# Performance work log

Measured on AMD Instinct MI355X. Metric: run time of the kernel, lower is better.

## Reference

```python
import jax, jax.numpy as jnp
import numpy as np

H, DH, D, S, B = 8, 64, 512, 512, 2
EPS = 1e-5

def _trop_linear(x, W):
    # y[..., o] = max_i (x[..., i] + W[o, i])
    return jnp.max(x[..., None, :] + W, axis=-1)

def _layer_norm(x, gamma, beta):
    mu = jnp.mean(x, axis=-1, keepdims=True)
    var = jnp.mean((x - mu) ** 2, axis=-1, keepdims=True)
    return (x - mu) * jax.lax.rsqrt(var + EPS) * gamma + beta

def setup_inputs() -> dict:
    key = jax.random.key(0)
    ks = jax.random.split(key, 8)
    sc = lambda fan_in: 1.0 / np.sqrt(fan_in)
    return {
        "h":   jax.random.normal(ks[0], (S, B, D), jnp.float32),
        "Wq":  jax.random.normal(ks[1], (H * DH, D), jnp.float32) * sc(D),
        "Wkv": jax.random.normal(ks[2], (2 * H * DH, D), jnp.float32) * sc(D),
        "Wqt": jax.random.normal(ks[3], (DH, DH), jnp.float32),
        "Wkt": jax.random.normal(ks[4], (DH, DH), jnp.float32),
        "Wvt": jax.random.normal(ks[5], (DH, DH), jnp.float32),
        "lam": jnp.ones((1, 1, D), jnp.float32),
        "Wo":  jax.random.normal(ks[6], (D, H * DH), jnp.float32) * sc(H * DH),
        "gamma": jnp.ones((D,), jnp.float32),
        "beta":  jnp.zeros((D,), jnp.float32),
    }

def reference(h, Wq, Wkv, Wqt, Wkt, Wvt, lam, Wo, gamma, beta):
    # h: [S, B, D]; mems=None so c == h; pre_lnorm=False
    c = h
    head_q = h @ Wq.T                                # [S, B, H*DH]
    kv = c @ Wkv.T                                   # [S, B, 2*H*DH]
    head_k, head_v = jnp.split(kv, 2, axis=-1)

    norm = lambda x: jnp.log1p(jax.nn.relu(x)) - lam  # tropical normalize
    head_q, head_k, head_v = norm(head_q), norm(head_k), norm(head_v)

    # [S,B,H,DH] -> [B,S,H,DH] -> flat reshape to [B*H, S, DH] (matches torch)
    to_bh = lambda x: jnp.transpose(x.reshape(S, B, H, DH), (1, 0, 2, 3)).reshape(B * H, S, DH)
    q = _trop_linear(to_bh(head_q), Wqt)
    k = _trop_linear(to_bh(head_k), Wkt)
    v = _trop_linear(to_bh(head_v), Wvt)

    # tropical distance score: -(max_d(q-k) - min_d(q-k)) over head dim
    diff = q[:, :, None, :] - k[:, None, :, :]        # [BH, Sq, Sk, DH]
    attn_scores = -(jnp.max(diff, axis=-1) - jnp.min(diff, axis=-1))  # [BH,Sq,Sk]

    # max-plus aggregation: context = max_sk(score + v)
    sum_sv = attn_scores[..., None] + v[:, None, :, :]  # [BH, Sq, Sk, DH]
    context = jnp.max(sum_sv, axis=2)                   # [BH, Sq, DH]

    # flat reshape back (matches torch), permute, expm1
    context = context.reshape(B, H, S, DH)
    context = jnp.transpose(context, (2, 0, 1, 3))      # [S, B, H, DH]
    context = jnp.expm1(context)
    attn_vec = context.reshape(S, B, H * DH)

    attn_out = attn_vec @ Wo.T                          # [S, B, D]
    return _layer_norm(h + attn_out, gamma, beta)
```

## Files before the change

### kernel.cpp

```cpp
#include <hip/hip_runtime.h>
#include <cmath>

typedef __attribute__((ext_vector_type(8))) __bf16 bf16x8;
typedef __attribute__((ext_vector_type(4))) float f32x4;

namespace {
constexpr int GP = 512;
constexpr int WS_Q = 0;
constexpr int WS_K = 524288;
constexpr int WS_V = 1048576;
}

__device__ inline unsigned short f2bf(float x) {
  union { float f; unsigned u; } v; v.f = x;
  unsigned r = v.u + 0x7fff + ((v.u >> 16) & 1);
  return (unsigned short)(r >> 16);
}

__device__ inline void cvt8_store(unsigned short* dst, float4 a, float4 b) {
  ushort4 lo, hi;
  lo.x = f2bf(a.x); lo.y = f2bf(a.y); lo.z = f2bf(a.z); lo.w = f2bf(a.w);
  hi.x = f2bf(b.x); hi.y = f2bf(b.y); hi.z = f2bf(b.z); hi.w = f2bf(b.w);
  *(ushort4*)dst = lo; *(ushort4*)(dst + 4) = hi;
}

__global__ __launch_bounds__(256) void k_gemm0t(const float* __restrict__ h,
    const float* __restrict__ Wq, const float* __restrict__ Wkv,
    const float* __restrict__ lam, const float* __restrict__ Wqt,
    const float* __restrict__ Wkt, const float* __restrict__ Wvt,
    float* __restrict__ qkv)
{
  __shared__ unsigned short As[64][72];
  __shared__ unsigned short Bs[64][72];
  __shared__ float Wl[64][65];
  __shared__ float nl[64][68];
  const int tid = threadIdx.x;
  const int bx = blockIdx.x;
  const int r0 = blockIdx.y * 64, c0 = bx * 64;
  const int which = c0 >> 9;
  const int hh = bx & 7;
  const float* Wt = (which == 0) ? Wqt : (which == 1) ? Wkt : Wvt;
  #pragma unroll
  for (int q = 0; q < 16; ++q) {
    int idx = q * 256 + tid;
    Wl[idx >> 6][idx & 63] = Wt[idx];
  }
  const int w = tid >> 6, l = tid & 63;
  const int wr = (w >> 1) * 32, wc = (w & 1) * 32;
  const int srow = tid >> 3, sk8 = (tid & 7) * 8;
  f32x4 acc[2][2] = {};
  for (int kk = 0; kk < 512; kk += 64) {
    __syncthreads();
    #pragma unroll
    for (int q2 = 0; q2 < 2; ++q2) {
      int row = srow + q2 * 32;
      const float* ap = &h[(r0 + row) * 512 + kk + sk8];
      cvt8_store(&As[row][sk8], *(const float4*)ap, *(const float4*)(ap + 4));
      int c = c0 + row;
      const float* wrp = (c < 512) ? (Wq + c * 512) : (Wkv + (c - 512) * 512);
      cvt8_store(&Bs[row][sk8], *(const float4*)&wrp[kk + sk8],
                 *(const float4*)&wrp[kk + sk8 + 4]);
    }
    __syncthreads();
    #pragma unroll
    for (int ks = 0; ks < 2; ++ks) {
      const int kc = ks * 32 + (l >> 4) * 8;
      bf16x8 a0 = *(const bf16x8*)&As[wr +      (l & 15)][kc];
      bf16x8 a1 = *(const bf16x8*)&As[wr + 16 + (l & 15)][kc];
      bf16x8 b0 = *(const bf16x8*)&Bs[wc +      (l & 15)][kc];
      bf16x8 b1 = *(const bf16x8*)&Bs[wc + 16 + (l & 15)][kc];
      acc[0][0] = __builtin_amdgcn_mfma_f32_16x16x32_bf16(a0, b0, acc[0][0], 0, 0, 0);
      acc[0][1] = __builtin_amdgcn_mfma_f32_16x16x32_bf16(a0, b1, acc[0][1], 0, 0, 0);
      acc[1][0] = __builtin_amdgcn_mfma_f32_16x16x32_bf16(a1, b0, acc[1][0], 0, 0, 0);
      acc[1][1] = __builtin_amdgcn_mfma_f32_16x16x32_bf16(a1, b1, acc[1][1], 0, 0, 0);
    }
  }
  #pragma unroll
  for (int i = 0; i < 2; ++i)
    #pragma unroll
    for (int j = 0; j < 2; ++j)
      #pragma unroll
      for (int r = 0; r < 4; ++r) {
        int rl = wr + i * 16 + (l >> 4) * 4 + r;
        int cl = wc + j * 16 + (l & 15);
        nl[rl][cl] = log1pf(fmaxf(acc[i][j][r], 0.f)) - lam[hh * 64 + cl];
      }
  __syncthreads();
  float wreg[64];
  #pragma unroll
  for (int i = 0; i < 64; ++i) wreg[i] = Wl[l][i];
  #pragma unroll 2
  for (int it = 0; it < 16; ++it) {
    int lr = w + it * 4;
    float m0 = -INFINITY, m1 = -INFINITY;
    #pragma unroll
    for (int i = 0; i < 64; i += 4) {
      f32x4 nv = *(const f32x4*)&nl[lr][i];
      float t0 = nv[0] + wreg[i],     t1 = nv[1] + wreg[i + 1];
      float t2 = nv[2] + wreg[i + 2], t3 = nv[3] + wreg[i + 3];
      m0 = fmaxf(fmaxf(m0, t0), t1);
      m1 = fmaxf(fmaxf(m1, t2), t3);
    }
    int r = r0 + lr;
    int s = r >> 1, bb = r & 1;
    int g = bb * 8 + (s >> 6);
    int p = ((s & 63) << 3) | hh;
    qkv[which * 524288 + ((g << 9) + p) * 64 + l] = fmaxf(m0, m1);
  }
}

__global__ __launch_bounds__(256) void k_attn(const float* __restrict__ qkv,
    float* __restrict__ ctxp)
{
  const int pt = blockIdx.x;
  const int g  = blockIdx.y;
  const int cs = blockIdx.z;
  const float* qb = qkv + WS_Q + g * GP * 64;
  const float* kb = qkv + WS_K + g * GP * 64;
  const float* vb = qkv + WS_V + g * GP * 64;
  __shared__ float qs[64][64];
  __shared__ float ks[64][64];
  __shared__ float vs[64][64];
  __shared__ float ss[64][68];
  const int tid = threadIdx.x;
  const int tr = tid >> 4, tc = tid & 15;
  #pragma unroll
  for (int q4 = 0; q4 < 4; ++q4) {
    int row = tr + q4 * 16;
    *(f32x4*)&qs[row][(tc ^ (row & 7)) * 4] =
        *(const f32x4*)&qb[(pt * 64 + row) * 64 + tc * 4];
  }
  float ctx[4][4];
  #pragma unroll
  for (int i = 0; i < 4; ++i)
    #pragma unroll
    for (int j = 0; j < 4; ++j) ctx[i][j] = -INFINITY;

  const int xq0 = (4 * tr) & 7;
  for (int cc = 0; cc < 2; ++cc) {
    const int c0 = cs * 128 + cc * 64;
    __syncthreads();
    #pragma unroll
    for (int q4 = 0; q4 < 4; ++q4) {
      int row = tr + q4 * 16;
      int sb = (tc ^ (row & 7)) * 4;
      *(f32x4*)&ks[row][sb] = *(const f32x4*)&kb[(c0 + row) * 64 + tc * 4];
      *(f32x4*)&vs[row][sb] = *(const f32x4*)&vb[(c0 + row) * 64 + tc * 4];
    }
    __syncthreads();
    float mx[4][4], mn[4][4];
    #pragma unroll
    for (int i = 0; i < 4; ++i)
      #pragma unroll
      for (int m = 0; m < 4; ++m) { mx[i][m] = -INFINITY; mn[i][m] = INFINITY; }
    #pragma unroll 4
    for (int b = 0; b < 16; ++b) {
      f32x4 qv[4], kv[4];
      #pragma unroll
      for (int i = 0; i < 4; ++i)
        qv[i] = *(const f32x4*)&qs[4 * tr + i][(b ^ ((xq0 + i) & 7)) * 4];
      const int kblk = (b ^ (tc & 7)) * 4;
      #pragma unroll
      for (int m = 0; m < 4; ++m)
        kv[m] = *(const f32x4*)&ks[tc + 16 * m][kblk];
      #pragma unroll
      for (int i = 0; i < 4; ++i)
        #pragma unroll
        for (int m = 0; m < 4; ++m) {
          float d0 = qv[i][0] - kv[m][0];
          float d1 = qv[i][1] - kv[m][1];
          float d2 = qv[i][2] - kv[m][2];
          float d3 = qv[i][3] - kv[m][3];
          mx[i][m] = fmaxf(fmaxf(mx[i][m], d0), d1);
          mn[i][m] = fminf(fminf(mn[i][m], d0), d1);
          mx[i][m] = fmaxf(fmaxf(mx[i][m], d2), d3);
          mn[i][m] = fminf(fminf(mn[i][m], d2), d3);
        }
    }
    #pragma unroll
    for (int i = 0; i < 4; ++i)
      #pragma unroll
      for (int m = 0; m < 4; ++m)
        ss[4 * tr + i][tc + 16 * m] = mn[i][m] - mx[i][m];
    __syncthreads();
    #pragma unroll 4
    for (int cb = 0; cb < 16; ++cb) {
      f32x4 sv[4], vv[4];
      #pragma unroll
      for (int i = 0; i < 4; ++i)
        sv[i] = *(const f32x4*)&ss[4 * tr + i][cb * 4];
      #pragma unroll
      for (int e = 0; e < 4; ++e) {
        int c = cb * 4 + e;
        vv[e] = *(const f32x4*)&vs[c][(tc ^ (c & 7)) * 4];
      }
      #pragma unroll
      for (int i = 0; i < 4; ++i) {
        #pragma unroll
        for (int j = 0; j < 4; ++j)
          ctx[i][j] = fmaxf(fmaxf(ctx[i][j], sv[i][0] + vv[0][j]),
                            sv[i][1] + vv[1][j]);
        #pragma unroll
        for (int j = 0; j < 4; ++j)
          ctx[i][j] = fmaxf(fmaxf(ctx[i][j], sv[i][2] + vv[2][j]),
                            sv[i][3] + vv[3][j]);
      }
    }
  }
  int base = cs * 524288 + g * 32768 + (pt * 64 + 4 * tr) * 64 + tc * 4;
  #pragma unroll
  for (int i = 0; i < 4; ++i) {
    f32x4 o;
    #pragma unroll
    for (int j = 0; j < 4; ++j) o[j] = ctx[i][j];
    *(f32x4*)&ctxp[base + i * 64] = o;
  }
}

__global__ __launch_bounds__(256) void k_gemm1c(const float* __restrict__ ctxp,
    const float* __restrict__ Wo, float* __restrict__ ao)
{
  __shared__ unsigned short As[64][72];
  __shared__ unsigned short Bs[64][72];
  const int tid = threadIdx.x;
  const int r0 = blockIdx.y * 64, c0 = blockIdx.x * 64;
  const int w = tid >> 6, l = tid & 63;
  const int wr = (w >> 1) * 32, wc = (w & 1) * 32;
  const int srow = tid >> 3, sk8 = (tid & 7) * 8;
  f32x4 acc[2][2] = {};
  for (int kk = 0; kk < 512; kk += 64) {
    __syncthreads();
    #pragma unroll
    for (int q2 = 0; q2 < 2; ++q2) {
      int row = srow + q2 * 32;
      int r = r0 + row;
      int p = r >> 1, b2 = r & 1;
      int j0 = kk + sk8;
      int h2 = j0 >> 6, d0 = j0 & 63;
      const float* cp = ctxp + (b2 * 8 + h2) * 32768 + p * 64 + d0;
      f32x4 m0 = *(const f32x4*)cp;
      f32x4 m1 = *(const f32x4*)(cp + 4);
      #pragma unroll
      for (int cs = 1; cs < 4; ++cs) {
        f32x4 a0 = *(const f32x4*)(cp + cs * 524288);
        f32x4 a1 = *(const f32x4*)(cp + cs * 524288 + 4);
        #pragma unroll
        for (int e = 0; e < 4; ++e) {
          m0[e] = fmaxf(m0[e], a0[e]);
          m1[e] = fmaxf(m1[e], a1[e]);
        }
      }
      ushort4 lo, hi;
      lo.x = f2bf(expm1f(m0[0])); lo.y = f2bf(expm1f(m0[1]));
      lo.z = f2bf(expm1f(m0[2])); lo.w = f2bf(expm1f(m0[3]));
      hi.x = f2bf(expm1f(m1[0])); hi.y = f2bf(expm1f(m1[1]));
      hi.z = f2bf(expm1f(m1[2])); hi.w = f2bf(expm1f(m1[3]));
      *(ushort4*)&As[row][sk8] = lo;
      *(ushort4*)&As[row][sk8 + 4] = hi;
      const float* bp = &Wo[(c0 + row) * 512 + kk + sk8];
      cvt8_store(&Bs[row][sk8], *(const float4*)bp, *(const float4*)(bp + 4));
    }
    __syncthreads();
    #pragma unroll
    for (int ks = 0; ks < 2; ++ks) {
      const int kc = ks * 32 + (l >> 4) * 8;
      bf16x8 a0 = *(const bf16x8*)&As[wr +      (l & 15)][kc];
      bf16x8 a1 = *(const bf16x8*)&As[wr + 16 + (l & 15)][kc];
      bf16x8 b0 = *(const bf16x8*)&Bs[wc +      (l & 15)][kc];
      bf16x8 b1 = *(const bf16x8*)&Bs[wc + 16 + (l & 15)][kc];
      acc[0][0] = __builtin_amdgcn_mfma_f32_16x16x32_bf16(a0, b0, acc[0][0], 0, 0, 0);
      acc[0][1] = __builtin_amdgcn_mfma_f32_16x16x32_bf16(a0, b1, acc[0][1], 0, 0, 0);
      acc[1][0] = __builtin_amdgcn_mfma_f32_16x16x32_bf16(a1, b0, acc[1][0], 0, 0, 0);
      acc[1][1] = __builtin_amdgcn_mfma_f32_16x16x32_bf16(a1, b1, acc[1][1], 0, 0, 0);
    }
  }
  #pragma unroll
  for (int i = 0; i < 2; ++i)
    #pragma unroll
    for (int j = 0; j < 2; ++j)
      #pragma unroll
      for (int r = 0; r < 4; ++r) {
        int row = r0 + wr + i * 16 + (l >> 4) * 4 + r;
        int col = c0 + wc + j * 16 + (l & 15);
        ao[row * 512 + col] = acc[i][j][r];
      }
}

__global__ __launch_bounds__(256) void k_ln(const float* __restrict__ hin,
    const float* __restrict__ ao, const float* __restrict__ gamma,
    const float* __restrict__ beta, float* __restrict__ outp)
{
  const int r = blockIdx.x * 4 + (threadIdx.x >> 6);
  const int lane = threadIdx.x & 63;
  const int c0 = lane * 8;
  f32x4 h0 = *(const f32x4*)&hin[r * 512 + c0];
  f32x4 h1 = *(const f32x4*)&hin[r * 512 + c0 + 4];
  f32x4 a0 = *(const f32x4*)&ao[r * 512 + c0];
  f32x4 a1 = *(const f32x4*)&ao[r * 512 + c0 + 4];
  float x[8];
  #pragma unroll
  for (int e = 0; e < 4; ++e) { x[e] = h0[e] + a0[e]; x[4 + e] = h1[e] + a1[e]; }
  float sum = 0.f, sq = 0.f;
  #pragma unroll
  for (int e = 0; e < 8; ++e) { sum += x[e]; sq += x[e] * x[e]; }
  #pragma unroll
  for (int o = 32; o > 0; o >>= 1) {
    sum += __shfl_xor(sum, o);
    sq  += __shfl_xor(sq, o);
  }
  float mu  = sum * (1.f / 512.f);
  float var = sq * (1.f / 512.f) - mu * mu;
  float rstd = rsqrtf(fmaxf(var, 0.f) + 1e-5f);
  f32x4 o0, o1;
  #pragma unroll
  for (int e = 0; e < 4; ++e) {
    o0[e] = (x[e]     - mu) * rstd * gamma[c0 + e]     + beta[c0 + e];
    o1[e] = (x[4 + e] - mu) * rstd * gamma[c0 + 4 + e] + beta[c0 + 4 + e];
  }
  *(f32x4*)&outp[r * 512 + c0]     = o0;
  *(f32x4*)&outp[r * 512 + c0 + 4] = o1;
}

extern "C" void kernel_launch(void* const* d_in, const int* in_sizes, int n_in,
                              void* d_out, int out_size, void* d_ws, size_t ws_size,
                              hipStream_t stream) {
  const float* hin   = (const float*)d_in[0];
  const float* Wq    = (const float*)d_in[1];
  const float* Wkv   = (const float*)d_in[2];
  const float* Wqt   = (const float*)d_in[3];
  const float* Wkt   = (const float*)d_in[4];
  const float* Wvt   = (const float*)d_in[5];
  const float* lam   = (const float*)d_in[6];
  const float* Wo    = (const float*)d_in[7];
  const float* gamma = (const float*)d_in[8];
  const float* beta  = (const float*)d_in[9];
  char* wsb = (char*)d_ws;
  float* qkvbuf = (float*)wsb;
  float* ctxp   = (float*)(wsb + 6291456);
  float* ao     = (float*)wsb;
  float* out    = (float*)d_out;

  k_gemm0t<<<dim3(24, 16),   256, 0, stream>>>(hin, Wq, Wkv, lam, Wqt, Wkt, Wvt, qkvbuf);
  k_attn  <<<dim3(8, 16, 4), 256, 0, stream>>>(qkvbuf, ctxp);
  k_gemm1c<<<dim3(8, 16),    256, 0, stream>>>(ctxp, Wo, ao);
  k_ln    <<<dim3(256),      256, 0, stream>>>(hin, ao, gamma, beta, out);
}
```

Before: 80.76 us.

## Run tropical attention in packed fp16 with 8-way key split

After: 103.7 us. +28.4%, slower.

```diff
diff --git a/kernel.cpp b/kernel.cpp
--- a/kernel.cpp
+++ b/kernel.cpp
@@ -3,12 +3,11 @@
 
 typedef __attribute__((ext_vector_type(8))) __bf16 bf16x8;
 typedef __attribute__((ext_vector_type(4))) float f32x4;
+typedef _Float16 f16;
+typedef __attribute__((ext_vector_type(2))) _Float16 f16x2;
 
 namespace {
 constexpr int GP = 512;
-constexpr int WS_Q = 0;
-constexpr int WS_K = 524288;
-constexpr int WS_V = 1048576;
 }
 
 __device__ inline unsigned short f2bf(float x) {
@@ -28,7 +27,7 @@
     const float* __restrict__ Wq, const float* __restrict__ Wkv,
     const float* __restrict__ lam, const float* __restrict__ Wqt,
     const float* __restrict__ Wkt, const float* __restrict__ Wvt,
-    float* __restrict__ qkv)
+    f16* __restrict__ qkvh)
 {
   __shared__ unsigned short As[64][72];
   __shared__ unsigned short Bs[64][72];
@@ -105,119 +104,125 @@
     int s = r >> 1, bb = r & 1;
     int g = bb * 8 + (s >> 6);
     int p = ((s & 63) << 3) | hh;
-    qkv[which * 524288 + ((g << 9) + p) * 64 + l] = fmaxf(m0, m1);
-  }
-}
-
-__global__ __launch_bounds__(256) void k_attn(const float* __restrict__ qkv,
-    float* __restrict__ ctxp)
+    qkvh[which * 524288 + ((g << 9) + p) * 64 + l] = (f16)fmaxf(m0, m1);
+  }
+}
+
+__global__ __launch_bounds__(256) void k_attn(const f16* __restrict__ qkv,
+    f16* __restrict__ ctxp)
 {
   const int pt = blockIdx.x;
   const int g  = blockIdx.y;
   const int cs = blockIdx.z;
-  const float* qb = qkv + WS_Q + g * GP * 64;
-  const float* kb = qkv + WS_K + g * GP * 64;
-  const float* vb = qkv + WS_V + g * GP * 64;
-  __shared__ float qs[64][64];
-  __shared__ float ks[64][64];
-  __shared__ float vs[64][64];
-  __shared__ float ss[64][68];
+  const f16* qb = qkv +           (size_t)g * GP * 64;
+  const f16* kb = qkv + 524288  + (size_t)g * GP * 64;
+  const f16* vb = qkv + 1048576 + (size_t)g * GP * 64;
+  __shared__ f16 qs[64][64];
+  __shared__ f16 ks[64][64];
+  __shared__ f16 vs[64][64];
+  __shared__ f16 ss[64][68];
   const int tid = threadIdx.x;
   const int tr = tid >> 4, tc = tid & 15;
-  #pragma unroll
-  for (int q4 = 0; q4 < 4; ++q4) {
-    int row = tr + q4 * 16;
-    *(f32x4*)&qs[row][(tc ^ (row & 7)) * 4] =
-        *(const f32x4*)&qb[(pt * 64 + row) * 64 + tc * 4];
-  }
-  float ctx[4][4];
+  {
+    int row = tid >> 3, blk = tid & 7;
+    int c0 = cs * 64;
+    #pragma unroll
+    for (int q2 = 0; q2 < 2; ++q2) {
+      int r = row + q2 * 32;
+      int sb = (blk ^ (r & 7)) * 8;
+      *(int4*)&qs[r][sb] = *(const int4*)&qb[(pt * 64 + r) * 64 + blk * 8];
+      *(int4*)&ks[r][sb] = *(const int4*)&kb[(c0 + r) * 64 + blk * 8];
+      *(int4*)&vs[r][sb] = *(const int4*)&vb[(c0 + r) * 64 + blk * 8];
+    }
+  }
+  __syncthreads();
+  const f16 NEGI = (f16)(-INFINITY);
+  const f16 POSI = (f16)(INFINITY);
+  const f16x2 NEG2 = { NEGI, NEGI };
+  const f16x2 POS2 = { POSI, POSI };
+  f16x2 mx2[4][4], mn2[4][4];
   #pragma unroll
   for (int i = 0; i < 4; ++i)
     #pragma unroll
-    for (int j = 0; j < 4; ++j) ctx[i][j] = -INFINITY;
-
-  const int xq0 = (4 * tr) & 7;
-  for (int cc = 0; cc < 2; ++cc) {
-    const int c0 = cs * 128 + cc * 64;
-    __syncthreads();
-    #pragma unroll
-    for (int q4 = 0; q4 < 4; ++q4) {
-      int row = tr + q4 * 16;
-      int sb = (tc ^ (row & 7)) * 4;
-      *(f32x4*)&ks[row][sb] = *(const f32x4*)&kb[(c0 + row) * 64 + tc * 4];
-      *(f32x4*)&vs[row][sb] = *(const f32x4*)&vb[(c0 + row) * 64 + tc * 4];
-    }
-    __syncthreads();
-    float mx[4][4], mn[4][4];
+    for (int m = 0; m < 4; ++m) { mx2[i][m] = NEG2; mn2[i][m] = POS2; }
+  #pragma unroll
+  for (int b = 0; b < 8; ++b) {
+    f16x2 qv[4][4], kv[4][4];
+    #pragma unroll
+    for (int i = 0; i < 4; ++i) {
+      int r = 4 * tr + i;
+      *(int4*)&qv[i][0] = *(const int4*)&qs[r][(b ^ (r & 7)) * 8];
+    }
+    #pragma unroll
+    for (int m = 0; m < 4; ++m)
+      *(int4*)&kv[m][0] = *(const int4*)&ks[tc + 16 * m][(b ^ (tc & 7)) * 8];
     #pragma unroll
     for (int i = 0; i < 4; ++i)
       #pragma unroll
-      for (int m = 0; m < 4; ++m) { mx[i][m] = -INFINITY; mn[i][m] = INFINITY; }
-    #pragma unroll 4
-    for (int b = 0; b < 16; ++b) {
-      f32x4 qv[4], kv[4];
-      #pragma unroll
-      for (int i = 0; i < 4; ++i)
-        qv[i] = *(const f32x4*)&qs[4 * tr + i][(b ^ ((xq0 + i) & 7)) * 4];
-      const int kblk = (b ^ (tc & 7)) * 4;
-      #pragma unroll
       for (int m = 0; m < 4; ++m)
-        kv[m] = *(const f32x4*)&ks[tc + 16 * m][kblk];
-      #pragma unroll
-      for (int i = 0; i < 4; ++i)
         #pragma unroll
-        for (int m = 0; m < 4; ++m) {
-          float d0 = qv[i][0] - kv[m][0];
-          float d1 = qv[i][1] - kv[m][1];
-          float d2 = qv[i][2] - kv[m][2];
-          float d3 = qv[i][3] - kv[m][3];
-          mx[i][m] = fmaxf(fmaxf(mx[i][m], d0), d1);
-          mn[i][m] = fminf(fminf(mn[i][m], d0), d1);
-          mx[i][m] = fmaxf(fmaxf(mx[i][m], d2), d3);
-          mn[i][m] = fminf(fminf(mn[i][m], d2), d3);
+        for (int e = 0; e < 4; ++e) {
+          f16x2 d = qv[i][e] - kv[m][e];
+          mx2[i][m] = __builtin_elementwise_max(mx2[i][m], d);
+          mn2[i][m] = __builtin_elementwise_min(mn2[i][m], d);
         }
-    }
-    #pragma unroll
-    for (int i = 0; i < 4; ++i)
-      #pragma unroll
-      for (int m = 0; m < 4; ++m)
-        ss[4 * tr + i][tc + 16 * m] = mn[i][m] - mx[i][m];
-    __syncthreads();
-    #pragma unroll 4
-    for (int cb = 0; cb < 16; ++cb) {
-      f32x4 sv[4], vv[4];
-      #pragma unroll
-      for (int i = 0; i < 4; ++i)
-        sv[i] = *(const f32x4*)&ss[4 * tr + i][cb * 4];
-      #pragma unroll
-      for (int e = 0; e < 4; ++e) {
-        int c = cb * 4 + e;
-        vv[e] = *(const f32x4*)&vs[c][(tc ^ (c & 7)) * 4];
-      }
+  }
+  #pragma unroll
+  for (int i = 0; i < 4; ++i)
+    #pragma unroll
+    for (int m = 0; m < 4; ++m) {
+      f16 mxv = (mx2[i][m][0] > mx2[i][m][1]) ? mx2[i][m][0] : mx2[i][m][1];
+      f16 mnv = (mn2[i][m][0] < mn2[i][m][1]) ? mn2[i][m][0] : mn2[i][m][1];
+      ss[tc + 16 * m][4 * tr + i] = mnv - mxv;
+    }
+  __syncthreads();
+  f16x2 ctx[4][4];
+  #pragma unroll
+  for (int i = 0; i < 4; ++i)
+    #pragma unroll
+    for (int j = 0; j < 4; ++j) ctx[i][j] = NEG2;
+  const int ch = tc >> 3, dg = tc & 7;
+  #pragma unroll
+  for (int gi = 0; gi < 4; ++gi) {
+    #pragma unroll
+    for (int e = 0; e < 8; ++e) {
+      int c = ch * 32 + gi * 8 + e;
+      f16x2 vv[4];
+      *(int4*)&vv[0] = *(const int4*)&vs[c][(dg ^ (c & 7)) * 8];
+      f16 sr[4];
+      *(int2*)&sr[0] = *(const int2*)&ss[c][4 * tr];
       #pragma unroll
       for (int i = 0; i < 4; ++i) {
+        f16x2 s2 = { sr[i], sr[i] };
         #pragma unroll
         for (int j = 0; j < 4; ++j)
-          ctx[i][j] = fmaxf(fmaxf(ctx[i][j], sv[i][0] + vv[0][j]),
-                            sv[i][1] + vv[1][j]);
-        #pragma unroll
-        for (int j = 0; j < 4; ++j)
-          ctx[i][j] = fmaxf(fmaxf(ctx[i][j], sv[i][2] + vv[2][j]),
-                            sv[i][3] + vv[3][j]);
+          ctx[i][j] = __builtin_elementwise_max(ctx[i][j], s2 + vv[j]);
       }
     }
   }
-  int base = cs * 524288 + g * 32768 + (pt * 64 + 4 * tr) * 64 + tc * 4;
-  #pragma unroll
-  for (int i = 0; i < 4; ++i) {
-    f32x4 o;
-    #pragma unroll
-    for (int j = 0; j < 4; ++j) o[j] = ctx[i][j];
-    *(f32x4*)&ctxp[base + i * 64] = o;
-  }
-}
-
-__global__ __launch_bounds__(256) void k_gemm1c(const float* __restrict__ ctxp,
+  #pragma unroll
+  for (int i = 0; i < 4; ++i)
+    #pragma unroll
+    for (int j = 0; j < 4; ++j) {
+      int o = __shfl_xor(*(int*)&ctx[i][j], 8);
+      ctx[i][j] = __builtin_elementwise_max(ctx[i][j], *(f16x2*)&o);
+    }
+  if (tc < 8) {
+    size_t base = (size_t)cs * 524288 + (size_t)g * 32768
+                + (size_t)(pt * 64 + 4 * tr) * 64 + dg * 8;
+    #pragma unroll
+    for (int i = 0; i < 4; ++i) {
+      int4 o;
+      ((f16x2*)&o)[0] = ctx[i][0];
+      ((f16x2*)&o)[1] = ctx[i][1];
+      ((f16x2*)&o)[2] = ctx[i][2];
+      ((f16x2*)&o)[3] = ctx[i][3];
+      *(int4*)&ctxp[base + i * 64] = o;
+    }
+  }
+}
+
+__global__ __launch_bounds__(256) void k_gemm1c(const f16* __restrict__ ctxp,
     const float* __restrict__ Wo, float* __restrict__ ao)
 {
   __shared__ unsigned short As[64][72];
@@ -236,25 +241,27 @@
       int r = r0 + row;
       int p = r >> 1, b2 = r & 1;
       int j0 = kk + sk8;
-      int h2 = j0 >> 6, d0 = j0 & 63;
-      const float* cp = ctxp + (b2 * 8 + h2) * 32768 + p * 64 + d0;
-      f32x4 m0 = *(const f32x4*)cp;
-      f32x4 m1 = *(const f32x4*)(cp + 4);
-      #pragma unroll
-      for (int cs = 1; cs < 4; ++cs) {
-        f32x4 a0 = *(const f32x4*)(cp + cs * 524288);
-        f32x4 a1 = *(const f32x4*)(cp + cs * 524288 + 4);
+      int h2i = j0 >> 6, d0 = j0 & 63;
+      const f16* cp = ctxp + (size_t)(b2 * 8 + h2i) * 32768 + p * 64 + d0;
+      f16x2 m[4];
+      *(int4*)&m[0] = *(const int4*)cp;
+      #pragma unroll
+      for (int cs2 = 1; cs2 < 8; ++cs2) {
+        f16x2 t[4];
+        *(int4*)&t[0] = *(const int4*)(cp + (size_t)cs2 * 524288);
         #pragma unroll
-        for (int e = 0; e < 4; ++e) {
-          m0[e] = fmaxf(m0[e], a0[e]);
-          m1[e] = fmaxf(m1[e], a1[e]);
-        }
+        for (int e = 0; e < 4; ++e)
+          m[e] = __builtin_elementwise_max(m[e], t[e]);
       }
       ushort4 lo, hi;
-      lo.x = f2bf(expm1f(m0[0])); lo.y = f2bf(expm1f(m0[1]));
-      lo.z = f2bf(expm1f(m0[2])); lo.w = f2bf(expm1f(m0[3]));
-      hi.x = f2bf(expm1f(m1[0])); hi.y = f2bf(expm1f(m1[1]));
-      hi.z = f2bf(expm1f(m1[2])); hi.w = f2bf(expm1f(m1[3]));
+      lo.x = f2bf(expm1f((float)m[0][0]));
+      lo.y = f2bf(expm1f((float)m[0][1]));
+      lo.z = f2bf(expm1f((float)m[1][0]));
+      lo.w = f2bf(expm1f((float)m[1][1]));
+      hi.x = f2bf(expm1f((float)m[2][0]));
+      hi.y = f2bf(expm1f((float)m[2][1]));
+      hi.z = f2bf(expm1f((float)m[3][0]));
+      hi.w = f2bf(expm1f((float)m[3][1]));
       *(ushort4*)&As[row][sk8] = lo;
       *(ushort4*)&As[row][sk8 + 4] = hi;
       const float* bp = &Wo[(c0 + row) * 512 + kk + sk8];
@@ -335,13 +342,13 @@
   const float* gamma = (const float*)d_in[8];
   const float* beta  = (const float*)d_in[9];
   char* wsb = (char*)d_ws;
-  float* qkvbuf = (float*)wsb;
-  float* ctxp   = (float*)(wsb + 6291456);
-  float* ao     = (float*)wsb;
-  float* out    = (float*)d_out;
-
-  k_gemm0t<<<dim3(24, 16),   256, 0, stream>>>(hin, Wq, Wkv, lam, Wqt, Wkt, Wvt, qkvbuf);
-  k_attn  <<<dim3(8, 16, 4), 256, 0, stream>>>(qkvbuf, ctxp);
+  f16*   qkvh = (f16*)wsb;
+  f16*   ctxp = (f16*)(wsb + 6291456);
+  float* ao   = (float*)wsb;
+  float* out  = (float*)d_out;
+
+  k_gemm0t<<<dim3(24, 16),   256, 0, stream>>>(hin, Wq, Wkv, lam, Wqt, Wkt, Wvt, qkvh);
+  k_attn  <<<dim3(8, 16, 8), 256, 0, stream>>>(qkvh, ctxp);
   k_gemm1c<<<dim3(8, 16),    256, 0, stream>>>(ctxp, Wo, ao);
   k_ln    <<<dim3(256),      256, 0, stream>>>(hin, ao, gamma, beta, out);
 }
```
